# Performance work log

Measured on AMD Instinct MI355X. Metric: run time of the kernel, lower is better.

## Reference

```python
import jax, jax.numpy as jnp
import numpy as np

N_NODES = 100000
N_EDGES = 1600000
D_FEAT = 256
HIDDEN = 256
OUT = 128


def _glorot(key, shape):
    fan_in, fan_out = shape[1], shape[0]
    lim = float(np.sqrt(6.0 / (fan_in + fan_out)))
    return jax.random.uniform(key, shape, jnp.float32, -lim, lim)


def setup_inputs() -> dict:
    key = jax.random.key(0)
    ks = jax.random.split(key, 12)
    x = jax.random.normal(ks[0], (N_NODES, D_FEAT), jnp.float32)
    edge_index = jax.random.randint(ks[1], (2, N_EDGES), 0, N_NODES, jnp.int64)
    return {
        "x": x,
        "edge_index": edge_index,
        # SAGEConv1: lin_l (neighbors, has bias), lin_r (root, no bias)
        "W1l": _glorot(ks[2], (HIDDEN, D_FEAT)),
        "b1l": jnp.zeros((HIDDEN,), jnp.float32),
        "W1r": _glorot(ks[3], (HIDDEN, D_FEAT)),
        # SAGEConv2
        "W2l": _glorot(ks[4], (OUT, HIDDEN)),
        "b2l": jnp.zeros((OUT,), jnp.float32),
        "W2r": _glorot(ks[5], (OUT, HIDDEN)),
        # EdgeDecoder
        "Wd1": _glorot(ks[6], (OUT, 2 * OUT)),
        "bd1": jnp.zeros((OUT,), jnp.float32),
        "Wd2": _glorot(ks[7], (1, OUT)),
        "bd2": jnp.zeros((1,), jnp.float32),
    }


def _sage_conv(x, src, dst, Wl, bl, Wr):
    # mean-aggregate source features into destination nodes (PyG SAGEConv, aggr='mean')
    msg_sum = jax.ops.segment_sum(x[src], dst, num_segments=N_NODES)  # [N, d]
    cnt = jax.ops.segment_sum(jnp.ones((src.shape[0],), x.dtype), dst, num_segments=N_NODES)
    mean = msg_sum / jnp.maximum(cnt, 1.0)[:, None]
    return mean @ Wl.T + bl + x @ Wr.T


def reference(x, edge_index, W1l, b1l, W1r, W2l, b2l, W2r, Wd1, bd1, Wd2, bd2):
    src, dst = edge_index[0], edge_index[1]
    # NodeEncoder
    h = jax.nn.relu(_sage_conv(x, src, dst, W1l, b1l, W1r))
    z = _sage_conv(h, src, dst, W2l, b2l, W2r)  # [N, OUT]
    # EdgeDecoder: gather per-edge endpoint embeddings, concat, MLP
    zc = jnp.concatenate([z[src], z[dst]], axis=-1)  # [E, 2*OUT]
    hd = jax.nn.relu(zc @ Wd1.T + bd1)
    out = hd @ Wd2.T + bd2  # [E, 1]
    return out.reshape(-1)
```

## Files before the change

### kernel.cpp

```cpp
#include <hip/hip_runtime.h>
#include <stdint.h>

static constexpr int NN = 100000;
static constexpr int NE = 1600000;
static constexpr int NB_SCAN = (NN + 255) / 256;
static constexpr int NB_CVTX = NN * 256 / 4 / 256;
static constexpr int NB_HIST = NE / 256;
static constexpr int NB_CVTW = 897;

typedef __bf16 bf16;
typedef __bf16 bf16x4 __attribute__((ext_vector_type(4)));
typedef __bf16 bf16x8 __attribute__((ext_vector_type(8)));
typedef float floatx4 __attribute__((ext_vector_type(4)));

__device__ __forceinline__ void async16(const void* g, void* l) {
  __builtin_amdgcn_global_load_lds(
      (const __attribute__((address_space(1))) void*)g,
      (__attribute__((address_space(3))) void*)l, 16, 0, 0);
}

__device__ __forceinline__ uint32_t pk4_fp8(float a, float b, float c, float d) {
  uint32_t v = 0;
  v = (uint32_t)__builtin_amdgcn_cvt_pk_fp8_f32(a, b, (int)v, false);
  v = (uint32_t)__builtin_amdgcn_cvt_pk_fp8_f32(c, d, (int)v, true);
  return v;
}

__device__ __forceinline__ void acc_fp8x8(float* a, uint2 v) {
  a[0] += __builtin_amdgcn_cvt_f32_fp8(v.x, 0);
  a[1] += __builtin_amdgcn_cvt_f32_fp8(v.x, 1);
  a[2] += __builtin_amdgcn_cvt_f32_fp8(v.x, 2);
  a[3] += __builtin_amdgcn_cvt_f32_fp8(v.x, 3);
  a[4] += __builtin_amdgcn_cvt_f32_fp8(v.y, 0);
  a[5] += __builtin_amdgcn_cvt_f32_fp8(v.y, 1);
  a[6] += __builtin_amdgcn_cvt_f32_fp8(v.y, 2);
  a[7] += __builtin_amdgcn_cvt_f32_fp8(v.y, 3);
}

__global__ void k_cvtx_hist(const float* __restrict__ x, bf16* __restrict__ xb,
                            uint32_t* __restrict__ xq,
                            const int* __restrict__ dst, int* __restrict__ cnt) {
  int b = blockIdx.x;
  if (b < NB_CVTX) {
    int t = b * 256 + threadIdx.x;
    const float4 v = ((const float4*)x)[t];
    bf16x4 o;
    o.x = (bf16)v.x; o.y = (bf16)v.y; o.z = (bf16)v.z; o.w = (bf16)v.w;
    ((bf16x4*)xb)[t] = o;
    xq[t] = pk4_fp8(v.x, v.y, v.z, v.w);
  } else {
    int e = (b - NB_CVTX) * 256 + threadIdx.x;
    atomicAdd(&cnt[dst[e]], 1);
  }
}

__global__ void k_cvtw_scanpart(
    const float* __restrict__ W1l, const float* __restrict__ W1r,
    const float* __restrict__ W2l, const float* __restrict__ W2r,
    const float* __restrict__ Wd1, const float* __restrict__ bd1,
    bf16* __restrict__ B1, bf16* __restrict__ B2,
    bf16* __restrict__ Bd, float* __restrict__ biasPQ,
    const int* __restrict__ cnt, int* __restrict__ part, int N) {
  int b = blockIdx.x;
  if (b < NB_CVTW) {
    int g = b * 256 + threadIdx.x;
    if (g < 131072) {
      int o = g >> 9, k = g & 511;
      float v = (k < 256) ? W1l[o * 256 + k] : W1r[o * 256 + k - 256];
      B1[g] = (bf16)v;
    } else if (g < 131072 + 65536) {
      int t = g - 131072;
      int o = t >> 8, k = t & 255;
      float v = (o < 128) ? W2l[o * 256 + k] : W2r[(o - 128) * 256 + k];
      B2[t] = (bf16)v;
    } else if (g < 131072 + 65536 + 32768) {
      int t = g - 196608;
      int o = t >> 7, k = t & 127;
      float v = (o < 128) ? Wd1[o * 256 + k] : Wd1[(o - 128) * 256 + 128 + k];
      Bd[t] = (bf16)v;
    } else if (g < 131072 + 65536 + 32768 + 256) {
      int t = g - 229376;
      biasPQ[t] = (t < 128) ? bd1[t] : 0.0f;
    }
  } else {
    __shared__ int sh[256];
    int bb = b - NB_CVTW;
    int t = threadIdx.x;
    int i = bb * 256 + t;
    sh[t] = (i < N) ? cnt[i] : 0;
    __syncthreads();
    for (int off = 128; off > 0; off >>= 1) {
      if (t < off) sh[t] += sh[t + off];
      __syncthreads();
    }
    if (t == 0) part[bb] = sh[0];
  }
}

__global__ __launch_bounds__(512) void k_scan_mid(int* __restrict__ part, int NB) {
  __shared__ int sh[512];
  int t = threadIdx.x;
  int v = (t < NB) ? part[t] : 0;
  sh[t] = v;
  __syncthreads();
  for (int off = 1; off < 512; off <<= 1) {
    int u = (t >= off) ? sh[t - off] : 0;
    __syncthreads();
    sh[t] += u;
    __syncthreads();
  }
  if (t < NB) part[t] = sh[t] - v;
}

__global__ void k_scan_fin(const int* __restrict__ cnt, const int* __restrict__ part,
                           int* __restrict__ rowptr, int N, int E) {
  __shared__ int sh[256];
  int t = threadIdx.x;
  int i = blockIdx.x * 256 + t;
  int v = (i < N) ? cnt[i] : 0;
  sh[t] = v;
  __syncthreads();
  for (int off = 1; off < 256; off <<= 1) {
    int u = (t >= off) ? sh[t - off] : 0;
    __syncthreads();
    sh[t] += u;
    __syncthreads();
  }
  if (i < N) rowptr[i] = part[blockIdx.x] + sh[t] - v;
  if (i == 0) rowptr[N] = E;
}

__global__ void k_fill(const int* __restrict__ src, const int* __restrict__ dst,
                       const int* __restrict__ rowptr, int* __restrict__ cursor,
                       int* __restrict__ csr, int* __restrict__ ceid, int E) {
  int e = blockIdx.x * 256 + threadIdx.x;
  if (e < E) {
    int d = dst[e];
    int pos = rowptr[d] + atomicAdd(&cursor[d], 1);
    csr[pos] = src[e];
    ceid[pos] = e;
  }
}

__global__ void k_agg(const uint8_t* __restrict__ xq, const int* __restrict__ rowptr,
                      const int* __restrict__ csr, bf16* __restrict__ mean) {
  int wave = threadIdx.x >> 6, lane = threadIdx.x & 63;
  int n = blockIdx.x * 4 + wave;
  int s = rowptr[n], e = rowptr[n + 1];
  int half = lane >> 5, l32 = lane & 31;
  float a[8] = {};
  const uint8_t* base = xq + l32 * 8;
  int i = s + half;
  for (; i + 6 < e; i += 8) {
    int c0 = csr[i], c1 = csr[i + 2], c2 = csr[i + 4], c3 = csr[i + 6];
    uint2 v0 = *(const uint2*)(base + (size_t)c0 * 256);
    uint2 v1 = *(const uint2*)(base + (size_t)c1 * 256);
    uint2 v2 = *(const uint2*)(base + (size_t)c2 * 256);
    uint2 v3 = *(const uint2*)(base + (size_t)c3 * 256);
    acc_fp8x8(a, v0); acc_fp8x8(a, v1); acc_fp8x8(a, v2); acc_fp8x8(a, v3);
  }
  for (; i < e; i += 2) {
    uint2 v = *(const uint2*)(base + (size_t)csr[i] * 256);
    acc_fp8x8(a, v);
  }
  int deg = e - s;
  float sc = 1.0f / (float)(deg > 0 ? deg : 1);
  bf16x8 o;
#pragma unroll
  for (int j = 0; j < 8; ++j) {
    float t = a[j] + __shfl_xor(a[j], 32);
    o[j] = (bf16)(t * sc);
  }
  if (half == 0)
    *(bf16x8*)(mean + (size_t)n * 256 + l32 * 8) = o;
}

__global__ void k_agg2z(const uint8_t* __restrict__ hq, const bf16* __restrict__ hr,
                        const int* __restrict__ rowptr, const int* __restrict__ csr,
                        const float* __restrict__ b2l, bf16* __restrict__ zf) {
  int wave = threadIdx.x >> 6, lane = threadIdx.x & 63;
  int n = blockIdx.x * 4 + wave;
  int s = rowptr[n], e = rowptr[n + 1];
  int sub = lane >> 4, l16 = lane & 15;
  float a[8] = {};
  const uint8_t* base = hq + l16 * 8;
  int i = s + sub;
  for (; i + 4 < e; i += 8) {
    int c0 = csr[i], c1 = csr[i + 4];
    uint2 v0 = *(const uint2*)(base + (size_t)c0 * 128);
    uint2 v1 = *(const uint2*)(base + (size_t)c1 * 128);
    acc_fp8x8(a, v0); acc_fp8x8(a, v1);
  }
  for (; i < e; i += 4) {
    uint2 v = *(const uint2*)(base + (size_t)csr[i] * 128);
    acc_fp8x8(a, v);
  }
  int deg = e - s;
  float sc = 1.0f / (float)(deg > 0 ? deg : 1);
  bf16x8 hv = *(const bf16x8*)(hr + (size_t)n * 128 + l16 * 8);
  const float4* b4 = (const float4*)(b2l + l16 * 8);
  float4 ba = b4[0], bb = b4[1];
  float bl[8] = {ba.x, ba.y, ba.z, ba.w, bb.x, bb.y, bb.z, bb.w};
  bf16x8 o;
#pragma unroll
  for (int j = 0; j < 8; ++j) {
    float t = a[j];
    t += __shfl_xor(t, 16);
    t += __shfl_xor(t, 32);
    o[j] = (bf16)(t * sc + (float)hv[j] + bl[j]);
  }
  if (sub == 0)
    *(bf16x8*)(zf + (size_t)n * 128 + l16 * 8) = o;
}

__global__ __launch_bounds__(256) void k_conv_gemm(
    const bf16* __restrict__ A1, const bf16* __restrict__ A2,
    const bf16* __restrict__ B, const float* __restrict__ bias,
    bf16* __restrict__ out, int Nrows) {
  __shared__ bf16 As[128 * 64];
  __shared__ bf16 Bs[128 * 64];
  const int tid = threadIdx.x, wave = tid >> 6, lane = tid & 63;
  const int quad = lane >> 4, l16 = lane & 15;
  const int rowBase = blockIdx.y * 128;
  const int colBase = blockIdx.x * 128;
  const int wr = (wave >> 1) * 64;
  const int wc = (wave & 1) * 64;
  floatx4 acc[4][4] = {};

  for (int kc = 0; kc < 8; ++kc) {
    const bf16* Asrc = (kc < 4) ? A1 : A2;
    const int kb = (kc & 3) * 64;
    for (int i = 0; i < 4; ++i) {
      int u = wave * 256 + i * 64 + lane;
      int row = u >> 3, seg = u & 7;
      int sg = seg ^ (row & 7);
      int node = rowBase + row;
      if (node >= Nrows) node = Nrows - 1;
      async16(Asrc + (size_t)node * 256 + kb + sg * 8, &As[(wave * 256 + i * 64) * 8]);
    }
    for (int i = 0; i < 4; ++i) {
      int u = wave * 256 + i * 64 + lane;
      int row = u >> 3, seg = u & 7;
      int sg = seg ^ (row & 7);
      async16(B + (size_t)(colBase + row) * 512 + kc * 64 + sg * 8,
              &Bs[(wave * 256 + i * 64) * 8]);
    }
    __syncthreads();
    for (int ks = 0; ks < 2; ++ks) {
      bf16x8 af[4], bq[4];
      const int sw = (ks * 4 + quad) ^ (l16 & 7);
      for (int mt = 0; mt < 4; ++mt)
        af[mt] = *(const bf16x8*)&As[(wr + mt * 16 + l16) * 64 + sw * 8];
      for (int nt = 0; nt < 4; ++nt)
        bq[nt] = *(const bf16x8*)&Bs[(wc + nt * 16 + l16) * 64 + sw * 8];
      for (int mt = 0; mt < 4; ++mt)
        for (int nt = 0; nt < 4; ++nt)
          acc[mt][nt] = __builtin_amdgcn_mfma_f32_16x16x32_bf16(af[mt], bq[nt], acc[mt][nt], 0, 0, 0);
    }
    __syncthreads();
  }
  float bv[4];
  for (int nt = 0; nt < 4; ++nt) bv[nt] = bias[colBase + wc + nt * 16 + l16];
  for (int mt = 0; mt < 4; ++mt)
    for (int nt = 0; nt < 4; ++nt) {
      int gcol = colBase + wc + nt * 16 + l16;
      for (int r = 0; r < 4; ++r) {
        int grow = rowBase + wr + mt * 16 + quad * 4 + r;
        if (grow < Nrows) {
          float v = fmaxf(acc[mt][nt][r] + bv[nt], 0.0f);
          out[(size_t)grow * 256 + gcol] = (bf16)v;
        }
      }
    }
}

template <int KDIM, int EPI>
__global__ __launch_bounds__(256) void k_gemm(
    const bf16* __restrict__ A, const bf16* __restrict__ B,
    const float* __restrict__ bias, void* __restrict__ out1,
    void* __restrict__ out2, int Nrows) {
  __shared__ bf16 As[128 * 64];
  __shared__ bf16 Bs[128 * 64];
  const int tid = threadIdx.x, wave = tid >> 6, lane = tid & 63;
  const int quad = lane >> 4, l16 = lane & 15;
  const int rowBase = blockIdx.y * 128;
  const int colBase = blockIdx.x * 128;
  const int wr = (wave >> 1) * 64;
  const int wc = (wave & 1) * 64;
  floatx4 acc[4][4] = {};

  for (int kc = 0; kc < KDIM / 64; ++kc) {
    for (int i = 0; i < 4; ++i) {
      int u = wave * 256 + i * 64 + lane;
      int row = u >> 3, seg = u & 7;
      int sg = seg ^ (row & 7);
      int node = rowBase + row;
      if (node >= Nrows) node = Nrows - 1;
      async16(A + (size_t)node * KDIM + kc * 64 + sg * 8, &As[(wave * 256 + i * 64) * 8]);
    }
    for (int i = 0; i < 4; ++i) {
      int u = wave * 256 + i * 64 + lane;
      int row = u >> 3, seg = u & 7;
      int sg = seg ^ (row & 7);
      async16(B + (size_t)(colBase + row) * KDIM + kc * 64 + sg * 8,
              &Bs[(wave * 256 + i * 64) * 8]);
    }
    __syncthreads();
    for (int ks = 0; ks < 2; ++ks) {
      bf16x8 af[4], bq[4];
      const int sw = (ks * 4 + quad) ^ (l16 & 7);
      for (int mt = 0; mt < 4; ++mt)
        af[mt] = *(const bf16x8*)&As[(wr + mt * 16 + l16) * 64 + sw * 8];
      for (int nt = 0; nt < 4; ++nt)
        bq[nt] = *(const bf16x8*)&Bs[(wc + nt * 16 + l16) * 64 + sw * 8];
      for (int mt = 0; mt < 4; ++mt)
        for (int nt = 0; nt < 4; ++nt)
          acc[mt][nt] = __builtin_amdgcn_mfma_f32_16x16x32_bf16(af[mt], bq[nt], acc[mt][nt], 0, 0, 0);
    }
    __syncthreads();
  }
  float bv[4];
  for (int nt = 0; nt < 4; ++nt)
    bv[nt] = (EPI == 2) ? bias[colBase + wc + nt * 16 + l16] : 0.0f;
  const bool lowHalf = (colBase == 0);
  for (int mt = 0; mt < 4; ++mt)
    for (int nt = 0; nt < 4; ++nt) {
      int gcol = colBase + wc + nt * 16 + l16;
      for (int r = 0; r < 4; ++r) {
        int grow = rowBase + wr + mt * 16 + quad * 4 + r;
        if (grow < Nrows) {
          float v = acc[mt][nt][r] + bv[nt];
          if (lowHalf) {
            if (EPI == 1) {
              uint32_t pk = (uint32_t)__builtin_amdgcn_cvt_pk_fp8_f32(v, v, 0, false);
              ((uint8_t*)out1)[(size_t)grow * 128 + gcol] = (uint8_t)pk;
            } else {
              ((bf16*)out1)[(size_t)grow * 128 + gcol] = (bf16)v;
            }
          } else {
            ((bf16*)out2)[(size_t)grow * 128 + gcol - 128] = (bf16)v;
          }
        }
      }
    }
}

__global__ __launch_bounds__(256) void k_edge(
    const bf16* __restrict__ P, const bf16* __restrict__ Q,
    const int* __restrict__ rowptr, const int* __restrict__ csr,
    const int* __restrict__ ceid,
    const float* __restrict__ wd2, const float* __restrict__ bd2,
    float* __restrict__ out) {
  int wave = threadIdx.x >> 6, lane = threadIdx.x & 63;
  int n = blockIdx.x * 4 + wave;
  int s = rowptr[n], e = rowptr[n + 1];
  int sub = lane >> 4, l16 = lane & 15;
  bf16x8 qv = *(const bf16x8*)(Q + (size_t)n * 128 + l16 * 8);
  float qf[8];
#pragma unroll
  for (int j = 0; j < 8; ++j) qf[j] = (float)qv[j];
  const float4* w4 = (const float4*)(wd2 + l16 * 8);
  float4 wa = w4[0], wb = w4[1];
  float w[8] = {wa.x, wa.y, wa.z, wa.w, wb.x, wb.y, wb.z, wb.w};
  const float bout = bd2[0];
  int i = s + sub;
  for (; i + 4 < e; i += 8) {
    int c0 = csr[i], e0 = ceid[i];
    int c1 = csr[i + 4], e1 = ceid[i + 4];
    bf16x8 p0 = *(const bf16x8*)(P + (size_t)c0 * 128 + l16 * 8);
    bf16x8 p1 = *(const bf16x8*)(P + (size_t)c1 * 128 + l16 * 8);
    float a0 = 0.f, a1 = 0.f;
#pragma unroll
    for (int j = 0; j < 8; ++j) {
      a0 += fmaxf((float)p0[j] + qf[j], 0.f) * w[j];
      a1 += fmaxf((float)p1[j] + qf[j], 0.f) * w[j];
    }
    a0 += __shfl_xor(a0, 1); a1 += __shfl_xor(a1, 1);
    a0 += __shfl_xor(a0, 2); a1 += __shfl_xor(a1, 2);
    a0 += __shfl_xor(a0, 4); a1 += __shfl_xor(a1, 4);
    a0 += __shfl_xor(a0, 8); a1 += __shfl_xor(a1, 8);
    if (l16 == 0) { out[e0] = a0 + bout; out[e1] = a1 + bout; }
  }
  for (; i < e; i += 4) {
    int c = csr[i], eid = ceid[i];
    bf16x8 p = *(const bf16x8*)(P + (size_t)c * 128 + l16 * 8);
    float a = 0.f;
#pragma unroll
    for (int j = 0; j < 8; ++j)
      a += fmaxf((float)p[j] + qf[j], 0.f) * w[j];
    a += __shfl_xor(a, 1);
    a += __shfl_xor(a, 2);
    a += __shfl_xor(a, 4);
    a += __shfl_xor(a, 8);
    if (l16 == 0) out[eid] = a + bout;
  }
}

extern "C" void kernel_launch(void* const* d_in, const int* in_sizes, int n_in,
                              void* d_out, int out_size, void* d_ws, size_t ws_size,
                              hipStream_t stream) {
  const float* x   = (const float*)d_in[0];
  const int*   ei  = (const int*)d_in[1];
  const float* W1l = (const float*)d_in[2];
  const float* b1l = (const float*)d_in[3];
  const float* W1r = (const float*)d_in[4];
  const float* W2l = (const float*)d_in[5];
  const float* b2l = (const float*)d_in[6];
  const float* W2r = (const float*)d_in[7];
  const float* Wd1 = (const float*)d_in[8];
  const float* bd1 = (const float*)d_in[9];
  const float* Wd2 = (const float*)d_in[10];
  const float* bd2 = (const float*)d_in[11];
  float* out = (float*)d_out;

  const int N = NN, E = NE;
  const int* srcv = ei;
  const int* dstv = ei + E;

  char* w = (char*)d_ws;
  size_t off = 0;
  auto take = [&](size_t bytes) {
    size_t o = off;
    off = (off + bytes + 255) & ~(size_t)255;
    return o;
  };
  int*      cnt    = (int*)(w + take((size_t)N * 4));
  int*      cursor = (int*)(w + take((size_t)N * 4));
  int*      rowptr = (int*)(w + take((size_t)(N + 1) * 4));
  int*      part   = (int*)(w + take((size_t)NB_SCAN * 4));
  int*      csr    = (int*)(w + take((size_t)E * 4));
  int*      ceid   = (int*)(w + take((size_t)E * 4));
  bf16*     xb     = (bf16*)(w + take((size_t)N * 256 * 2));
  uint8_t*  xq     = (uint8_t*)(w + take((size_t)N * 256));
  bf16*     mean   = (bf16*)(w + take((size_t)N * 256 * 2));
  bf16*     h      = (bf16*)(w + take((size_t)N * 256 * 2));
  bf16*     zf     = (bf16*)(w + take((size_t)N * 128 * 2));
  bf16*     B1     = (bf16*)(w + take((size_t)131072 * 2));
  bf16*     B2     = (bf16*)(w + take((size_t)65536 * 2));
  bf16*     Bd     = (bf16*)(w + take((size_t)32768 * 2));
  float*    biasPQ = (float*)(w + take((size_t)256 * 4));
  uint8_t* hq = (uint8_t*)mean;
  bf16*    hr = (bf16*)(hq + (size_t)N * 128);
  bf16*    P  = h;
  bf16*    Q  = h + (size_t)N * 128;
  (void)ws_size; (void)n_in; (void)in_sizes; (void)out_size;

  hipMemsetAsync(cnt, 0, (size_t)((char*)rowptr - (char*)cnt), stream);

  k_cvtx_hist<<<NB_CVTX + NB_HIST, 256, 0, stream>>>(x, xb, (uint32_t*)xq, dstv, cnt);
  k_cvtw_scanpart<<<NB_CVTW + NB_SCAN, 256, 0, stream>>>(
      W1l, W1r, W2l, W2r, Wd1, bd1, B1, B2, Bd, biasPQ, cnt, part, N);
  k_scan_mid<<<1, 512, 0, stream>>>(part, NB_SCAN);
  k_scan_fin<<<NB_SCAN, 256, 0, stream>>>(cnt, part, rowptr, N, E);
  k_fill<<<E / 256, 256, 0, stream>>>(srcv, dstv, rowptr, cursor, csr, ceid, E);

  k_agg<<<N / 4, 256, 0, stream>>>(xq, rowptr, csr, mean);
  k_conv_gemm<<<dim3(2, 782), 256, 0, stream>>>(mean, xb, B1, b1l, h, N);
  k_gemm<256, 1><<<dim3(2, 782), 256, 0, stream>>>(h, B2, nullptr, hq, hr, N);
  k_agg2z<<<N / 4, 256, 0, stream>>>(hq, hr, rowptr, csr, b2l, zf);
  k_gemm<128, 2><<<dim3(2, 782), 256, 0, stream>>>(zf, Bd, biasPQ, P, Q, N);
  k_edge<<<N / 4, 256, 0, stream>>>(P, Q, rowptr, csr, ceid, Wd2, bd2, out);
}
```

Measured before the change: 666.6 us.

## Record histogram rank to drop fill atomics and CSR edge-id array

The histogram pass now saves each edge's atomicAdd return value as a 16-bit rank. The CSR fill then places edges with rowptr+rank instead of a second atomic cursor, and no longer writes the edge-id array. The edge kernel writes results in CSR order, and a new permutation kernel scatters them back to original edge order. Histogram and conversion blocks are also interleaved in the grid (4 convert : 1 histogram). This trades the fill atomics and ceid traffic for an extra rank array, an extra kernel launch, and a gather over outCSR.

```diff
diff --git a/kernel.cpp b/kernel.cpp
--- a/kernel.cpp
+++ b/kernel.cpp
@@ -39,18 +39,23 @@
 
 __global__ void k_cvtx_hist(const float* __restrict__ x, bf16* __restrict__ xb,
                             uint32_t* __restrict__ xq,
-                            const int* __restrict__ dst, int* __restrict__ cnt) {
+                            const int* __restrict__ dst, int* __restrict__ cnt,
+                            uint16_t* __restrict__ rank) {
   int b = blockIdx.x;
-  if (b < NB_CVTX) {
-    int t = b * 256 + threadIdx.x;
+  int m = b % 5;
+  if (m < 4) {
+    int cb = (b / 5) * 4 + m;
+    int t = cb * 256 + threadIdx.x;
     const float4 v = ((const float4*)x)[t];
     bf16x4 o;
     o.x = (bf16)v.x; o.y = (bf16)v.y; o.z = (bf16)v.z; o.w = (bf16)v.w;
     ((bf16x4*)xb)[t] = o;
     xq[t] = pk4_fp8(v.x, v.y, v.z, v.w);
   } else {
-    int e = (b - NB_CVTX) * 256 + threadIdx.x;
-    atomicAdd(&cnt[dst[e]], 1);
+    int hb = b / 5;
+    int e = hb * 256 + threadIdx.x;
+    int old = atomicAdd(&cnt[dst[e]], 1);
+    rank[e] = (uint16_t)old;
   }
 }
 
@@ -131,14 +136,14 @@
 }
 
 __global__ void k_fill(const int* __restrict__ src, const int* __restrict__ dst,
-                       const int* __restrict__ rowptr, int* __restrict__ cursor,
-                       int* __restrict__ csr, int* __restrict__ ceid, int E) {
+                       const int* __restrict__ rowptr,
+                       const uint16_t* __restrict__ rank,
+                       int* __restrict__ csr, int E) {
   int e = blockIdx.x * 256 + threadIdx.x;
   if (e < E) {
     int d = dst[e];
-    int pos = rowptr[d] + atomicAdd(&cursor[d], 1);
+    int pos = rowptr[d] + (int)rank[e];
     csr[pos] = src[e];
-    ceid[pos] = e;
   }
 }
 
@@ -348,9 +353,8 @@
 __global__ __launch_bounds__(256) void k_edge(
     const bf16* __restrict__ P, const bf16* __restrict__ Q,
     const int* __restrict__ rowptr, const int* __restrict__ csr,
-    const int* __restrict__ ceid,
     const float* __restrict__ wd2, const float* __restrict__ bd2,
-    float* __restrict__ out) {
+    float* __restrict__ outCSR) {
   int wave = threadIdx.x >> 6, lane = threadIdx.x & 63;
   int n = blockIdx.x * 4 + wave;
   int s = rowptr[n], e = rowptr[n + 1];
@@ -365,8 +369,7 @@
   const float bout = bd2[0];
   int i = s + sub;
   for (; i + 4 < e; i += 8) {
-    int c0 = csr[i], e0 = ceid[i];
-    int c1 = csr[i + 4], e1 = ceid[i + 4];
+    int c0 = csr[i], c1 = csr[i + 4];
     bf16x8 p0 = *(const bf16x8*)(P + (size_t)c0 * 128 + l16 * 8);
     bf16x8 p1 = *(const bf16x8*)(P + (size_t)c1 * 128 + l16 * 8);
     float a0 = 0.f, a1 = 0.f;
@@ -379,10 +382,10 @@
     a0 += __shfl_xor(a0, 2); a1 += __shfl_xor(a1, 2);
     a0 += __shfl_xor(a0, 4); a1 += __shfl_xor(a1, 4);
     a0 += __shfl_xor(a0, 8); a1 += __shfl_xor(a1, 8);
-    if (l16 == 0) { out[e0] = a0 + bout; out[e1] = a1 + bout; }
+    if (l16 == 0) { outCSR[i] = a0 + bout; outCSR[i + 4] = a1 + bout; }
   }
   for (; i < e; i += 4) {
-    int c = csr[i], eid = ceid[i];
+    int c = csr[i];
     bf16x8 p = *(const bf16x8*)(P + (size_t)c * 128 + l16 * 8);
     float a = 0.f;
 #pragma unroll
@@ -392,7 +395,17 @@
     a += __shfl_xor(a, 2);
     a += __shfl_xor(a, 4);
     a += __shfl_xor(a, 8);
-    if (l16 == 0) out[eid] = a + bout;
+    if (l16 == 0) outCSR[i] = a + bout;
+  }
+}
+
+__global__ void k_perm(const int* __restrict__ dst, const uint16_t* __restrict__ rank,
+                       const int* __restrict__ rowptr, const float* __restrict__ outCSR,
+                       float* __restrict__ out, int E) {
+  int e = blockIdx.x * 256 + threadIdx.x;
+  if (e < E) {
+    int d = dst[e];
+    out[e] = outCSR[rowptr[d] + (int)rank[e]];
   }
 }
 
@@ -425,11 +438,11 @@
     return o;
   };
   int*      cnt    = (int*)(w + take((size_t)N * 4));
-  int*      cursor = (int*)(w + take((size_t)N * 4));
   int*      rowptr = (int*)(w + take((size_t)(N + 1) * 4));
   int*      part   = (int*)(w + take((size_t)NB_SCAN * 4));
+  uint16_t* rank   = (uint16_t*)(w + take((size_t)E * 2));
   int*      csr    = (int*)(w + take((size_t)E * 4));
-  int*      ceid   = (int*)(w + take((size_t)E * 4));
+  float*    outCSR = (float*)(w + take((size_t)E * 4));
   bf16*     xb     = (bf16*)(w + take((size_t)N * 256 * 2));
   uint8_t*  xq     = (uint8_t*)(w + take((size_t)N * 256));
   bf16*     mean   = (bf16*)(w + take((size_t)N * 256 * 2));
@@ -445,19 +458,20 @@
   bf16*    Q  = h + (size_t)N * 128;
   (void)ws_size; (void)n_in; (void)in_sizes; (void)out_size;
 
-  hipMemsetAsync(cnt, 0, (size_t)((char*)rowptr - (char*)cnt), stream);
-
-  k_cvtx_hist<<<NB_CVTX + NB_HIST, 256, 0, stream>>>(x, xb, (uint32_t*)xq, dstv, cnt);
+  hipMemsetAsync(cnt, 0, (size_t)N * 4, stream);
+
+  k_cvtx_hist<<<NB_CVTX + NB_HIST, 256, 0, stream>>>(x, xb, (uint32_t*)xq, dstv, cnt, rank);
   k_cvtw_scanpart<<<NB_CVTW + NB_SCAN, 256, 0, stream>>>(
       W1l, W1r, W2l, W2r, Wd1, bd1, B1, B2, Bd, biasPQ, cnt, part, N);
   k_scan_mid<<<1, 512, 0, stream>>>(part, NB_SCAN);
   k_scan_fin<<<NB_SCAN, 256, 0, stream>>>(cnt, part, rowptr, N, E);
-  k_fill<<<E / 256, 256, 0, stream>>>(srcv, dstv, rowptr, cursor, csr, ceid, E);
+  k_fill<<<E / 256, 256, 0, stream>>>(srcv, dstv, rowptr, rank, csr, E);
 
   k_agg<<<N / 4, 256, 0, stream>>>(xq, rowptr, csr, mean);
   k_conv_gemm<<<dim3(2, 782), 256, 0, stream>>>(mean, xb, B1, b1l, h, N);
   k_gemm<256, 1><<<dim3(2, 782), 256, 0, stream>>>(h, B2, nullptr, hq, hr, N);
   k_agg2z<<<N / 4, 256, 0, stream>>>(hq, hr, rowptr, csr, b2l, zf);
   k_gemm<128, 2><<<dim3(2, 782), 256, 0, stream>>>(zf, Bd, biasPQ, P, Q, N);
-  k_edge<<<N / 4, 256, 0, stream>>>(P, Q, rowptr, csr, ceid, Wd2, bd2, out);
-}
+  k_edge<<<N / 4, 256, 0, stream>>>(P, Q, rowptr, csr, Wd2, bd2, outCSR);
+  k_perm<<<E / 256, 256, 0, stream>>>(dstv, rank, rowptr, outCSR, out, E);
+}
```

Measured after the change: 576.0 us. 1.16x faster.
